# Performance work log

Measured on AMD Instinct MI355X. Metric: run time of the kernel, lower is better.

The kernel has to match this reference:

```python
import jax, jax.numpy as jnp
import numpy as np

EPS = 1e-06


def setup_inputs() -> dict:
    key = jax.random.key(0)
    k1, k2 = jax.random.split(key)
    x = jax.random.normal(k1, (8, 128, 256, 256), dtype=jnp.float32)
    weights = jax.random.normal(k2, (128,), dtype=jnp.float32)
    return {"x": x, "weights": weights}


def reference(x, weights):
    # x: [b, q, h, w]; weights: [q]
    q = weights.shape[0]
    norm_const = jnp.float32(q)
    # use_cumsum=False path: softmax over features, scaled by norm_const
    wt = jax.nn.softmax(weights) * norm_const  # [q]
    # rank[b,i,h,w] = rank of x[b,i,h,w] when sorting dim 1 descending
    order = jnp.argsort(-x, axis=1)            # descending argsort
    rank = jnp.argsort(order, axis=1)          # inverse permutation -> ranks
    # gather per-rank weight and apply 1/sqrt(x^2 + eps)
    return wt[rank] * jax.lax.rsqrt(x * x + jnp.float32(EPS))
```

## Files before the change

kernel.cpp:

```cpp
#include <hip/hip_runtime.h>
#include <math.h>


#define Q    128
#define TCOL 64
#define HW   65536
#define EPSF 1e-6f

__device__ __forceinline__ int f2key(int b) {
    return b ^ (int)(((unsigned)(b >> 31)) >> 1);
}

__device__ __forceinline__ unsigned pack4(int a, int b, int c, int d) {
    return (unsigned)a | ((unsigned)b << 8) | ((unsigned)c << 16) | ((unsigned)d << 24);
}

__device__ __forceinline__ void tile16(int (*lk)[TCOL], unsigned (*lc)[TCOL],
                                       const int c, const int X0, const int NQ,
                                       const int Y0) {
    int kY[16], cY[16];
    #pragma unroll
    for (int u = 0; u < 16; ++u) kY[u] = lk[Y0 + u][c];
    #pragma unroll
    for (int u = 0; u < 16; ++u) cY[u] = NQ << 2;
    for (int m = 0; m < NQ; ++m) {
        const int xr  = X0 + (m << 2);
        const int kx0 = lk[xr + 0][c];
        const int kx1 = lk[xr + 1][c];
        const int kx2 = lk[xr + 2][c];
        const int kx3 = lk[xr + 3][c];
        int cx0 = 0, cx1 = 0, cx2 = 0, cx3 = 0;
        #pragma unroll
        for (int j = 0; j < 16; ++j) {
            const int ky = kY[j];
            const int s0 = (kx0 - ky) >> 31; cx0 -= s0;
            const int s1 = (kx1 - ky) >> 31; cx1 -= s1;
            const int s2 = (kx2 - ky) >> 31; cx2 -= s2;
            const int s3 = (kx3 - ky) >> 31; cx3 -= s3;
            cY[j] += (s0 + s1) + (s2 + s3);
        }
        atomicAdd(&lc[xr >> 2][c], pack4(cx0, cx1, cx2, cx3));
    }
    #pragma unroll
    for (int n = 0; n < 4; ++n)
        atomicAdd(&lc[(Y0 >> 2) + n][c],
                  pack4(cY[4 * n], cY[4 * n + 1], cY[4 * n + 2], cY[4 * n + 3]));
}

__device__ __forceinline__ void subdiag16(int (*lk)[TCOL], unsigned (*lc)[TCOL],
                                          const int c, const int B0) {
    int kD[16], cD[16];
    #pragma unroll
    for (int u = 0; u < 16; ++u) kD[u] = lk[B0 + u][c];
    #pragma unroll
    for (int u = 0; u < 16; ++u) cD[u] = u;
    #pragma unroll
    for (int a = 0; a < 16; ++a) {
        #pragma unroll
        for (int e = a + 1; e < 16; ++e) {
            const int s = (kD[a] - kD[e]) >> 31;
            cD[a] -= s;
            cD[e] += s;
        }
    }
    #pragma unroll
    for (int n = 0; n < 4; ++n)
        atomicAdd(&lc[(B0 >> 2) + n][c],
                  pack4(cD[4 * n], cD[4 * n + 1], cD[4 * n + 2], cD[4 * n + 3]));
}

__launch_bounds__(256, 4)
__global__ void rank_weight_kernel(const float* __restrict__ x,
                                   const float* __restrict__ weights,
                                   float* __restrict__ out) {
    __shared__ int      lds_k[Q][TCOL];
    __shared__ unsigned lds_cnt[Q / 4][TCOL];

    const int tid = threadIdx.x;
    const int g   = blockIdx.x;
    const int b   = g >> 10;
    const int hw0 = (g & 1023) << 6;
    const float* xb = x   + (size_t)b * Q * HW + hw0;
    float*       ob = out + (size_t)b * Q * HW + hw0;

    for (int f = tid; f < Q * (TCOL / 4); f += 256) {
        const int r = f >> 4;
        const int p = (f & 15) << 2;
        float4 v = *reinterpret_cast<const float4*>(xb + (size_t)r * HW + p);
        int4 k;
        k.x = f2key(__float_as_int(v.x));
        k.y = f2key(__float_as_int(v.y));
        k.z = f2key(__float_as_int(v.z));
        k.w = f2key(__float_as_int(v.w));
        *reinterpret_cast<int4*>(&lds_k[r][p]) = k;
    }
    {
        uint4 z = {0u, 0u, 0u, 0u};
        for (int i = tid; i < (Q / 4) * TCOL / 4; i += 256)
            reinterpret_cast<uint4*>(&lds_cnt[0][0])[i] = z;
    }

    const int wave = tid >> 6;
    const int c    = tid & 63;

    float w0s, w1s;
    {
        float a0 = weights[c], a1 = weights[c + 64];
        float m = fmaxf(a0, a1);
        #pragma unroll
        for (int off = 32; off; off >>= 1) m = fmaxf(m, __shfl_xor(m, off, 64));
        float e0 = __expf(a0 - m), e1 = __expf(a1 - m);
        float s = e0 + e1;
        #pragma unroll
        for (int off = 32; off; off >>= 1) s += __shfl_xor(s, off, 64);
        const float scale = 128.0f / s;
        w0s = e0 * scale;
        w1s = e1 * scale;
    }
    __syncthreads();

    const int B0 = wave << 5;

    subdiag16(lds_k, lds_cnt, c, B0);
    subdiag16(lds_k, lds_cnt, c, B0 + 16);
    tile16(lds_k, lds_cnt, c, B0, 4, B0 + 16);

    const int cXb = (wave == 3) ? 0  : (wave << 5);
    const int cYb = (wave == 3) ? 96 : ((wave << 5) + 32);
    tile16(lds_k, lds_cnt, c, cXb, 8, cYb);
    tile16(lds_k, lds_cnt, c, cXb, 8, cYb + 16);

    const int hXb = wave << 4;
    const int hYb = (wave < 2) ? 64 : 96;
    tile16(lds_k, lds_cnt, c, hXb, 4, hYb);
    tile16(lds_k, lds_cnt, c, hXb, 4, hYb + 16);

    __syncthreads();

    const int R0 = wave << 5;
    #pragma unroll
    for (int mw = 0; mw < 8; ++mw) {
        const unsigned wv = lds_cnt[(R0 >> 2) + mw][c];
        #pragma unroll
        for (int q = 0; q < 4; ++q) {
            const int   r    = R0 + (mw << 2) + q;
            const int   rank = (wv >> (q << 3)) & 0xFF;
            const int   k    = lds_k[r][c];
            const float xv   = __int_as_float(f2key(k));
            const int   rl   = rank & 63;
            const float wa   = __shfl(w0s, rl, 64);
            const float wb   = __shfl(w1s, rl, 64);
            const float wt   = (rank & 64) ? wb : wa;
            ob[(size_t)r * HW + c] = wt * rsqrtf(xv * xv + EPSF);
        }
    }
}

extern "C" void kernel_launch(void* const* d_in, const int* in_sizes, int n_in,
                              void* d_out, int out_size, void* d_ws, size_t ws_size,
                              hipStream_t stream) {
    const float* x  = (const float*)d_in[0];
    const float* wt = (const float*)d_in[1];
    float* out      = (float*)d_out;

    dim3 grid(8192), block(256);
    hipLaunchKernelGGL(rank_weight_kernel, grid, block, 0, stream, x, wt, out);
}
```

Baseline: 695.3 us.

## Compare raw floats directly and retile pairwise rank counting into 8x8 blocks

Drops the float-to-ordered-int key transform and compares float values directly with v_cmp-style selects, so LDS holds the raw inputs and the output stage no longer converts back. The pairwise comparison tiles are restructured from 4x16 strips into 8x8 blocks built from 4x4 micro-tiles, with a different accumulation and atomic pattern. Float comparison can differ from the integer key ordering for NaNs and signed zeros, and the new tiling issues more LDS atomics per comparison.

```diff
diff --git a/kernel.cpp b/kernel.cpp
--- a/kernel.cpp
+++ b/kernel.cpp
@@ -7,73 +7,77 @@
 #define HW   65536
 #define EPSF 1e-6f
 
-__device__ __forceinline__ int f2key(int b) {
-    return b ^ (int)(((unsigned)(b >> 31)) >> 1);
-}
-
 __device__ __forceinline__ unsigned pack4(int a, int b, int c, int d) {
     return (unsigned)a | ((unsigned)b << 8) | ((unsigned)c << 16) | ((unsigned)d << 24);
 }
 
-__device__ __forceinline__ void tile16(int (*lk)[TCOL], unsigned (*lc)[TCOL],
-                                       const int c, const int X0, const int NQ,
-                                       const int Y0) {
-    int kY[16], cY[16];
+__device__ __forceinline__ void mt44(const float* vx, int* ncx,
+                                     const float* vy, int* cy) {
+    int s[4][4];
     #pragma unroll
-    for (int u = 0; u < 16; ++u) kY[u] = lk[Y0 + u][c];
-    #pragma unroll
-    for (int u = 0; u < 16; ++u) cY[u] = NQ << 2;
-    for (int m = 0; m < NQ; ++m) {
-        const int xr  = X0 + (m << 2);
-        const int kx0 = lk[xr + 0][c];
-        const int kx1 = lk[xr + 1][c];
-        const int kx2 = lk[xr + 2][c];
-        const int kx3 = lk[xr + 3][c];
-        int cx0 = 0, cx1 = 0, cx2 = 0, cx3 = 0;
+    for (int k = 0; k < 4; ++k) {
         #pragma unroll
-        for (int j = 0; j < 16; ++j) {
-            const int ky = kY[j];
-            const int s0 = (kx0 - ky) >> 31; cx0 -= s0;
-            const int s1 = (kx1 - ky) >> 31; cx1 -= s1;
-            const int s2 = (kx2 - ky) >> 31; cx2 -= s2;
-            const int s3 = (kx3 - ky) >> 31; cx3 -= s3;
-            cY[j] += (s0 + s1) + (s2 + s3);
-        }
-        atomicAdd(&lc[xr >> 2][c], pack4(cx0, cx1, cx2, cx3));
+        for (int j = 0; j < 4; ++j)
+            s[k][j] = (vy[j] > vx[k]) ? -1 : 0;
     }
     #pragma unroll
-    for (int n = 0; n < 4; ++n)
-        atomicAdd(&lc[(Y0 >> 2) + n][c],
-                  pack4(cY[4 * n], cY[4 * n + 1], cY[4 * n + 2], cY[4 * n + 3]));
+    for (int k = 0; k < 4; ++k)
+        ncx[k] += (s[k][0] + s[k][1] + s[k][2]) + s[k][3];
+    #pragma unroll
+    for (int j = 0; j < 4; ++j)
+        cy[j]  += (s[0][j] + s[1][j] + s[2][j]) + s[3][j];
 }
 
-__device__ __forceinline__ void subdiag16(int (*lk)[TCOL], unsigned (*lc)[TCOL],
-                                          const int c, const int B0) {
-    int kD[16], cD[16];
+__device__ __forceinline__ void job(const float (*lv)[TCOL], unsigned (*lc)[TCOL],
+                                    const int c, const int X0, const int NX,
+                                    const int Y0, const int NY) {
+    for (int xo = 0; xo < NX; xo += 8) {
+        float vx[8]; int ncx[8];
+        #pragma unroll
+        for (int k = 0; k < 8; ++k) { vx[k] = lv[X0 + xo + k][c]; ncx[k] = 0; }
+        for (int yc = 0; yc < NY; yc += 8) {
+            float vy[8]; int cy[8];
+            #pragma unroll
+            for (int j = 0; j < 8; ++j) { vy[j] = lv[Y0 + yc + j][c]; cy[j] = 8; }
+            mt44(vx,     ncx,     vy,     cy);
+            mt44(vx,     ncx,     vy + 4, cy + 4);
+            mt44(vx + 4, ncx + 4, vy,     cy);
+            mt44(vx + 4, ncx + 4, vy + 4, cy + 4);
+            const int yw = (Y0 + yc) >> 2;
+            atomicAdd(&lc[yw][c],     pack4(cy[0], cy[1], cy[2], cy[3]));
+            atomicAdd(&lc[yw + 1][c], pack4(cy[4], cy[5], cy[6], cy[7]));
+        }
+        const int xw = (X0 + xo) >> 2;
+        atomicAdd(&lc[xw][c],     pack4(-ncx[0], -ncx[1], -ncx[2], -ncx[3]));
+        atomicAdd(&lc[xw + 1][c], pack4(-ncx[4], -ncx[5], -ncx[6], -ncx[7]));
+    }
+}
+
+__device__ __forceinline__ void tri16(const float (*lv)[TCOL], unsigned (*lc)[TCOL],
+                                      const int c, const int B0) {
+    float v[16]; int cd[16];
     #pragma unroll
-    for (int u = 0; u < 16; ++u) kD[u] = lk[B0 + u][c];
-    #pragma unroll
-    for (int u = 0; u < 16; ++u) cD[u] = u;
+    for (int u = 0; u < 16; ++u) { v[u] = lv[B0 + u][c]; cd[u] = u; }
     #pragma unroll
     for (int a = 0; a < 16; ++a) {
         #pragma unroll
         for (int e = a + 1; e < 16; ++e) {
-            const int s = (kD[a] - kD[e]) >> 31;
-            cD[a] -= s;
-            cD[e] += s;
+            const int s = (v[e] > v[a]) ? -1 : 0;
+            cd[a] -= s;
+            cd[e] += s;
         }
     }
     #pragma unroll
     for (int n = 0; n < 4; ++n)
         atomicAdd(&lc[(B0 >> 2) + n][c],
-                  pack4(cD[4 * n], cD[4 * n + 1], cD[4 * n + 2], cD[4 * n + 3]));
+                  pack4(cd[4 * n], cd[4 * n + 1], cd[4 * n + 2], cd[4 * n + 3]));
 }
 
 __launch_bounds__(256, 4)
 __global__ void rank_weight_kernel(const float* __restrict__ x,
                                    const float* __restrict__ weights,
                                    float* __restrict__ out) {
-    __shared__ int      lds_k[Q][TCOL];
+    __shared__ float    lds_v[Q][TCOL];
     __shared__ unsigned lds_cnt[Q / 4][TCOL];
 
     const int tid = threadIdx.x;
@@ -87,12 +91,7 @@
         const int r = f >> 4;
         const int p = (f & 15) << 2;
         float4 v = *reinterpret_cast<const float4*>(xb + (size_t)r * HW + p);
-        int4 k;
-        k.x = f2key(__float_as_int(v.x));
-        k.y = f2key(__float_as_int(v.y));
-        k.z = f2key(__float_as_int(v.z));
-        k.w = f2key(__float_as_int(v.w));
-        *reinterpret_cast<int4*>(&lds_k[r][p]) = k;
+        *reinterpret_cast<float4*>(&lds_v[r][p]) = v;
     }
     {
         uint4 z = {0u, 0u, 0u, 0u};
@@ -121,19 +120,17 @@
 
     const int B0 = wave << 5;
 
-    subdiag16(lds_k, lds_cnt, c, B0);
-    subdiag16(lds_k, lds_cnt, c, B0 + 16);
-    tile16(lds_k, lds_cnt, c, B0, 4, B0 + 16);
+    tri16(lds_v, lds_cnt, c, B0);
+    tri16(lds_v, lds_cnt, c, B0 + 16);
+    job(lds_v, lds_cnt, c, B0, 16, B0 + 16, 16);
 
     const int cXb = (wave == 3) ? 0  : (wave << 5);
     const int cYb = (wave == 3) ? 96 : ((wave << 5) + 32);
-    tile16(lds_k, lds_cnt, c, cXb, 8, cYb);
-    tile16(lds_k, lds_cnt, c, cXb, 8, cYb + 16);
+    job(lds_v, lds_cnt, c, cXb, 32, cYb, 32);
 
     const int hXb = wave << 4;
     const int hYb = (wave < 2) ? 64 : 96;
-    tile16(lds_k, lds_cnt, c, hXb, 4, hYb);
-    tile16(lds_k, lds_cnt, c, hXb, 4, hYb + 16);
+    job(lds_v, lds_cnt, c, hXb, 16, hYb, 32);
 
     __syncthreads();
 
@@ -145,8 +142,7 @@
         for (int q = 0; q < 4; ++q) {
             const int   r    = R0 + (mw << 2) + q;
             const int   rank = (wv >> (q << 3)) & 0xFF;
-            const int   k    = lds_k[r][c];
-            const float xv   = __int_as_float(f2key(k));
+            const float xv   = lds_v[r][c];
             const int   rl   = rank & 63;
             const float wa   = __shfl(w0s, rl, 64);
             const float wb   = __shfl(w1s, rl, 64);
```

Result: no change. 698.7 us (+0.5%).
